# Kernel tuning notes

Hardware: AMD Instinct MI355X
Metric: run time of the kernel (lower is better)

The kernel has to match this reference:

```python
import jax, jax.numpy as jnp
import numpy as np

WINDOW = 11
C1 = 0.01 ** 2
C2 = 0.03 ** 2
PAD = WINDOW // 2


def _box_filter(img, kernel):
    # img: [B,1,H,W], kernel: [1,1,w,w]; SAME padding (odd window)
    return jax.lax.conv_general_dilated(
        img, kernel,
        window_strides=(1, 1),
        padding=[(PAD, PAD), (PAD, PAD)],
        dimension_numbers=('NCHW', 'OIHW', 'NCHW'))


def setup_inputs() -> dict:
    key = jax.random.key(0)
    kx, ky = jax.random.split(key)
    B, C, H, W = 64, 1, 512, 512
    x = jax.random.uniform(kx, (B, C, H, W), dtype=jnp.float32)
    y = jax.random.uniform(ky, (B, C, H, W), dtype=jnp.float32)
    kernel = jnp.ones((1, 1, WINDOW, WINDOW), dtype=jnp.float32) / (WINDOW ** 2)
    return {"x": x, "y": y, "kernel": kernel}


def reference(x, y, kernel):
    mu_x = _box_filter(x, kernel)
    mu_y = _box_filter(y, kernel)
    mu_x2 = mu_x * mu_x
    mu_y2 = mu_y * mu_y
    mu_xy = mu_x * mu_y
    sigma_x2 = _box_filter(x * x, kernel) - mu_x2
    sigma_y2 = _box_filter(y * y, kernel) - mu_y2
    sigma_xy = _box_filter(x * y, kernel) - mu_xy
    ssim_map = ((2.0 * mu_xy + C1) * (2.0 * sigma_xy + C2)) / (
        (mu_x2 + mu_y2 + C1) * (sigma_x2 + sigma_y2 + C2))
    return 1.0 - jnp.mean(ssim_map)
```

## Files before the change

kernel.cpp:

```cpp
#include <hip/hip_runtime.h>
#include <stdint.h>


#define IMG_H 512
#define IMG_W 512
#define N_IMG 64
#define BAND  64
#define NBANDG 8
#define NBLOCKS (N_IMG * NBANDG)
#define NSLOT 19

#define SLOT_BYTES 4128
#define X1_OFF 1040
#define Y0_OFF 2064
#define Y1_OFF 3104

#define C1S2 1.4641f
#define C2S2 13.1769f

typedef __attribute__((address_space(3))) uint32_t lds_u32_t;
typedef const __attribute__((address_space(1))) uint32_t glb_u32_t;

__device__ __forceinline__ void dma16(void* lds, const void* g) {
    __builtin_amdgcn_global_load_lds((glb_u32_t*)g, (lds_u32_t*)lds, 16, 0, 0);
}

__device__ __forceinline__ float dpp_shr1(float v) {
    return __int_as_float(__builtin_amdgcn_update_dpp(
        0, __float_as_int(v), 0x138, 0xF, 0xF, true));
}
__device__ __forceinline__ float dpp_shl1(float v) {
    return __int_as_float(__builtin_amdgcn_update_dpp(
        0, __float_as_int(v), 0x130, 0xF, 0xF, true));
}

__device__ __forceinline__ int wrapS(int s) { return s >= NSLOT ? s - NSLOT : s; }

__global__ __launch_bounds__(128) void ssim_fused(const float* __restrict__ x,
                                                  const float* __restrict__ y,
                                                  float* __restrict__ part)
{
    __shared__ __align__(16) char ring[NSLOT][SLOT_BYTES];

    const int tx = threadIdx.x & 63;
    const int wv = threadIdx.x >> 6;
    const int lo = tx * 32 + ((tx & 32) >> 1);

    const int wid = (blockIdx.x & 7) * (NBLOCKS / 8) + (blockIdx.x >> 3);
    const int img = wid >> 3;
    const int bg  = wid & (NBANDG - 1);
    const int r0  = bg * BAND;

    const float* __restrict__ xi = x + (size_t)img * (IMG_H * IMG_W);
    const float* __restrict__ yi = y + (size_t)img * (IMG_H * IMG_W);

    auto dma_row = [&](int slot, int ri) {
        int rc = ri < 0 ? 0 : (ri > IMG_H - 1 ? IMG_H - 1 : ri);
        char* s = &ring[slot][0];
        const char* xg = (const char*)(xi + (size_t)rc * IMG_W) + tx * 16;
        const char* yg = (const char*)(yi + (size_t)rc * IMG_W) + tx * 16;
        dma16(s,          xg);
        dma16(s + X1_OFF, xg + 1024);
        dma16(s + Y0_OFF, yg);
        dma16(s + Y1_OFF, yg + 1024);
    };

    float Vx[8], Vy[8], Vss[8], Vxy[8];
#pragma unroll
    for (int j = 0; j < 8; ++j) { Vx[j] = 0.f; Vy[j] = 0.f; Vss[j] = 0.f; Vxy[j] = 0.f; }

    auto accum_add = [&](const char* s) {
        const float4* xr = (const float4*)(s + lo);
        const float4* yr = (const float4*)(s + Y0_OFF + lo);
        float4 x0 = xr[0], x1 = xr[1];
        float4 y0 = yr[0], y1 = yr[1];
        float xs[8] = {x0.x, x0.y, x0.z, x0.w, x1.x, x1.y, x1.z, x1.w};
        float ys[8] = {y0.x, y0.y, y0.z, y0.w, y1.x, y1.y, y1.z, y1.w};
#pragma unroll
        for (int j = 0; j < 8; ++j) {
            Vx[j] += xs[j];
            Vy[j] += ys[j];
            Vss[j] = fmaf(xs[j], xs[j], Vss[j]);
            Vss[j] = fmaf(ys[j], ys[j], Vss[j]);
            Vxy[j] = fmaf(xs[j], ys[j], Vxy[j]);
        }
    };

    auto accum_sub = [&](const char* s) {
        const float4* xr = (const float4*)(s + lo);
        const float4* yr = (const float4*)(s + Y0_OFF + lo);
        float4 x0 = xr[0], x1 = xr[1];
        float4 y0 = yr[0], y1 = yr[1];
        float xs[8] = {x0.x, x0.y, x0.z, x0.w, x1.x, x1.y, x1.z, x1.w};
        float ys[8] = {y0.x, y0.y, y0.z, y0.w, y1.x, y1.y, y1.z, y1.w};
#pragma unroll
        for (int j = 0; j < 8; ++j) {
            Vx[j]  -= xs[j];
            Vy[j]  -= ys[j];
            Vss[j] = fmaf(-xs[j], xs[j], Vss[j]);
            Vss[j] = fmaf(-ys[j], ys[j], Vss[j]);
            Vxy[j] = fmaf(-xs[j], ys[j], Vxy[j]);
        }
    };

    auto hsum = [&](const float (&V)[8], float (&S)[8]) {
        float w[18];
#pragma unroll
        for (int k = 0; k < 5; ++k) w[k] = dpp_shr1(V[3 + k]);
#pragma unroll
        for (int j = 0; j < 8; ++j) w[5 + j] = V[j];
#pragma unroll
        for (int k = 0; k < 5; ++k) w[13 + k] = dpp_shl1(V[k]);
        float s0 = (w[0] + w[1]) + (w[2] + w[3]);
        float s1 = (w[4] + w[5]) + (w[6] + w[7]);
        float s2 = (w[8] + w[9]) + w[10];
        float s  = (s0 + s1) + s2;
        S[0] = s;
#pragma unroll
        for (int j = 1; j < 8; ++j) { s += w[j + 10] - w[j - 1]; S[j] = s; }
    };

    auto ssim8 = [&](const float (&Sx)[8], const float (&Sy)[8],
                     const float (&Sss)[8], const float (&Sxy)[8],
                     float& loss) {
#pragma unroll
        for (int j = 0; j < 8; ++j) {
            float A  = Sx[j] * Sy[j];
            float B  = fmaf(Sx[j], Sx[j], Sy[j] * Sy[j]);
            float n1 = fmaf(A, 2.0f, C1S2);
            float n2 = fmaf(Sxy[j], 242.0f, fmaf(A, -2.0f, C2S2));
            float d1 = B + C1S2;
            float d2 = fmaf(Sss[j], 121.0f, C2S2 - B);
            loss += __fdividef(n1 * n2, d1 * d2);
        }
    };

#pragma unroll 1
    for (int k = wv; k < 16; k += 2) dma_row(k, r0 - 7 + k);
    __syncthreads();
#pragma unroll 1
    for (int t = 0; t < 11; ++t) {
        int row = r0 + wv - 7 + t;
        if (row >= 0) accum_add(&ring[wv + t][0]);
    }

    float loss = 0.0f;
    int cA = 11 + wv;
    int cS = wv;
    int cP = 16;
    const int po0 = 1 - wv;
    const int po1 = 3 - wv;

#pragma unroll 1
    for (int i = 0; i < BAND / 4; ++i) {
        const int base = r0 + 4 * i;
        const int a = base + wv;

        if (a + 4 < IMG_H) accum_add(&ring[cA][0]);
        if (a + 5 < IMG_H) accum_add(&ring[wrapS(cA + 1)][0]);
        if (a - 7 >= 0)    accum_sub(&ring[cS][0]);
        if (a - 6 >= 0)    accum_sub(&ring[wrapS(cS + 1)][0]);

        float Sx[8], Sy[8], Sss[8], Sxy[8];
        hsum(Vx, Sx); hsum(Vy, Sy); hsum(Vss, Sss); hsum(Vxy, Sxy);

        if (a + 6 < IMG_H) accum_add(&ring[wrapS(cA + 2)][0]);
        if (a + 7 < IMG_H) accum_add(&ring[wrapS(cA + 3)][0]);
        if (a - 5 >= 0)    accum_sub(&ring[wrapS(cS + 2)][0]);
        if (a - 4 >= 0)    accum_sub(&ring[wrapS(cS + 3)][0]);

        if (i < BAND / 4 - 1) {
            dma_row(wrapS(cP + po0), base + 9 + po0);
            dma_row(wrapS(cP + po1), base + 9 + po1);
        }

        ssim8(Sx, Sy, Sss, Sxy, loss);

        float Tx[8], Ty[8], Tss[8], Txy[8];
        hsum(Vx, Tx); hsum(Vy, Ty); hsum(Vss, Tss); hsum(Vxy, Txy);
        ssim8(Tx, Ty, Tss, Txy, loss);

        cA = wrapS(cA + 4); cS = wrapS(cS + 4); cP = wrapS(cP + 4);
        __syncthreads();
    }

#pragma unroll
    for (int off = 32; off > 0; off >>= 1)
        loss += __shfl_down(loss, off, 64);

    float* pr = reinterpret_cast<float*>(&ring[0][0]);
    if (tx == 0) pr[wv] = loss;
    __syncthreads();
    if (threadIdx.x == 0)
        part[blockIdx.x] = pr[0] + pr[1];
}

__global__ __launch_bounds__(256) void ssim_reduce(const float* __restrict__ part,
                                                   float* __restrict__ out)
{
    const int t  = threadIdx.x;
    const int tx = t & 63;
    float s = part[t] + part[t + 256];
#pragma unroll
    for (int off = 32; off > 0; off >>= 1)
        s += __shfl_down(s, off, 64);
    __shared__ float ws[4];
    if (tx == 0) ws[t >> 6] = s;
    __syncthreads();
    if (t == 0) {
        float total = (ws[0] + ws[1]) + (ws[2] + ws[3]);
        out[0] = 1.0f - total * (1.0f / ((float)N_IMG * IMG_H * IMG_W));
    }
}

extern "C" void kernel_launch(void* const* d_in, const int* in_sizes, int n_in,
                              void* d_out, int out_size, void* d_ws, size_t ws_size,
                              hipStream_t stream) {
    const float* x = (const float*)d_in[0];
    const float* y = (const float*)d_in[1];
    float* part = (float*)d_ws;

    ssim_fused<<<NBLOCKS, 128, 0, stream>>>(x, y, part);
    ssim_reduce<<<1, 256, 0, stream>>>(part, (float*)d_out);
}
```

Measured before the change: 158.2 us.

## Use three wavefronts per block, each advancing one output row per step

The fused SSIM kernel grows from two to three wavefronts per block. Each wave now keeps a separate running column sum for every third row and emits one output row per 3-row step, where before each wave handled two rows per 4-row step. The ring slots lose their padding and the per-lane skew offset, so LDS reads become plain tx*32 strides. The aim is more waves in flight and a simpler schedule; the risks are LDS bank conflicts from the unpadded layout, more redundant add/sub work per output row, and idle waves in the final step.

```diff
diff --git a/kernel.cpp b/kernel.cpp
--- a/kernel.cpp
+++ b/kernel.cpp
@@ -9,11 +9,10 @@
 #define NBANDG 8
 #define NBLOCKS (N_IMG * NBANDG)
 #define NSLOT 19
-
-#define SLOT_BYTES 4128
-#define X1_OFF 1040
-#define Y0_OFF 2064
-#define Y1_OFF 3104
+#define NSTEP 22
+
+#define SLOT_BYTES 4096
+#define Y0_OFF 2048
 
 #define C1S2 1.4641f
 #define C2S2 13.1769f
@@ -36,7 +35,7 @@
 
 __device__ __forceinline__ int wrapS(int s) { return s >= NSLOT ? s - NSLOT : s; }
 
-__global__ __launch_bounds__(128) void ssim_fused(const float* __restrict__ x,
+__global__ __launch_bounds__(192) void ssim_fused(const float* __restrict__ x,
                                                   const float* __restrict__ y,
                                                   float* __restrict__ part)
 {
@@ -44,12 +43,12 @@
 
     const int tx = threadIdx.x & 63;
     const int wv = threadIdx.x >> 6;
-    const int lo = tx * 32 + ((tx & 32) >> 1);
 
     const int wid = (blockIdx.x & 7) * (NBLOCKS / 8) + (blockIdx.x >> 3);
     const int img = wid >> 3;
     const int bg  = wid & (NBANDG - 1);
     const int r0  = bg * BAND;
+    const int q0  = r0 + wv;
 
     const float* __restrict__ xi = x + (size_t)img * (IMG_H * IMG_W);
     const float* __restrict__ yi = y + (size_t)img * (IMG_H * IMG_W);
@@ -60,9 +59,9 @@
         const char* xg = (const char*)(xi + (size_t)rc * IMG_W) + tx * 16;
         const char* yg = (const char*)(yi + (size_t)rc * IMG_W) + tx * 16;
         dma16(s,          xg);
-        dma16(s + X1_OFF, xg + 1024);
+        dma16(s + 1024,   xg + 1024);
         dma16(s + Y0_OFF, yg);
-        dma16(s + Y1_OFF, yg + 1024);
+        dma16(s + Y0_OFF + 1024, yg + 1024);
     };
 
     float Vx[8], Vy[8], Vss[8], Vxy[8];
@@ -70,8 +69,8 @@
     for (int j = 0; j < 8; ++j) { Vx[j] = 0.f; Vy[j] = 0.f; Vss[j] = 0.f; Vxy[j] = 0.f; }
 
     auto accum_add = [&](const char* s) {
-        const float4* xr = (const float4*)(s + lo);
-        const float4* yr = (const float4*)(s + Y0_OFF + lo);
+        const float4* xr = (const float4*)(s + (size_t)tx * 32);
+        const float4* yr = (const float4*)(s + Y0_OFF + (size_t)tx * 32);
         float4 x0 = xr[0], x1 = xr[1];
         float4 y0 = yr[0], y1 = yr[1];
         float xs[8] = {x0.x, x0.y, x0.z, x0.w, x1.x, x1.y, x1.z, x1.w};
@@ -87,8 +86,8 @@
     };
 
     auto accum_sub = [&](const char* s) {
-        const float4* xr = (const float4*)(s + lo);
-        const float4* yr = (const float4*)(s + Y0_OFF + lo);
+        const float4* xr = (const float4*)(s + (size_t)tx * 32);
+        const float4* yr = (const float4*)(s + Y0_OFF + (size_t)tx * 32);
         float4 x0 = xr[0], x1 = xr[1];
         float4 y0 = yr[0], y1 = yr[1];
         float xs[8] = {x0.x, x0.y, x0.z, x0.w, x1.x, x1.y, x1.z, x1.w};
@@ -136,51 +135,41 @@
     };
 
 #pragma unroll 1
-    for (int k = wv; k < 16; k += 2) dma_row(k, r0 - 7 + k);
+    for (int k = wv; k < 16; k += 3) dma_row(k + 1, r0 - 8 + k);
     __syncthreads();
 #pragma unroll 1
     for (int t = 0; t < 11; ++t) {
-        int row = r0 + wv - 7 + t;
-        if (row >= 0) accum_add(&ring[wv + t][0]);
+        int row = q0 - 8 + t;
+        if (row >= 0) accum_add(&ring[wv + 1 + t][0]);
     }
 
     float loss = 0.0f;
-    int cA = 11 + wv;
-    int cS = wv;
-    int cP = 16;
-    const int po0 = 1 - wv;
-    const int po1 = 3 - wv;
+    int c = 0;
 
 #pragma unroll 1
-    for (int i = 0; i < BAND / 4; ++i) {
-        const int base = r0 + 4 * i;
-        const int a = base + wv;
-
-        if (a + 4 < IMG_H) accum_add(&ring[cA][0]);
-        if (a + 5 < IMG_H) accum_add(&ring[wrapS(cA + 1)][0]);
-        if (a - 7 >= 0)    accum_sub(&ring[cS][0]);
-        if (a - 6 >= 0)    accum_sub(&ring[wrapS(cS + 1)][0]);
-
-        float Sx[8], Sy[8], Sss[8], Sxy[8];
-        hsum(Vx, Sx); hsum(Vy, Sy); hsum(Vss, Sss); hsum(Vxy, Sxy);
-
-        if (a + 6 < IMG_H) accum_add(&ring[wrapS(cA + 2)][0]);
-        if (a + 7 < IMG_H) accum_add(&ring[wrapS(cA + 3)][0]);
-        if (a - 5 >= 0)    accum_sub(&ring[wrapS(cS + 2)][0]);
-        if (a - 4 >= 0)    accum_sub(&ring[wrapS(cS + 3)][0]);
-
-        if (i < BAND / 4 - 1) {
-            dma_row(wrapS(cP + po0), base + 9 + po0);
-            dma_row(wrapS(cP + po1), base + 9 + po1);
-        }
-
-        ssim8(Sx, Sy, Sss, Sxy, loss);
-
-        float Tx[8], Ty[8], Tss[8], Txy[8];
-        hsum(Vx, Tx); hsum(Vy, Ty); hsum(Vss, Tss); hsum(Vxy, Txy);
-        ssim8(Tx, Ty, Tss, Txy, loss);
-
-        cA = wrapS(cA + 4); cS = wrapS(cS + 4); cP = wrapS(cP + 4);
+    for (int i = 0; i < NSTEP; ++i) {
+        const int base = r0 + 3 * i;
+        const int q = base + wv;
+        const bool act = (3 * i + wv) < BAND;
+
+        if (act) {
+            if (q - 8 >= 0) accum_sub(&ring[wrapS(c + 1 + wv)][0]);
+            if (q - 7 >= 0) accum_sub(&ring[wrapS(c + 2 + wv)][0]);
+            if (q - 6 >= 0) accum_sub(&ring[wrapS(c + 3 + wv)][0]);
+            if (q + 3 < IMG_H) accum_add(&ring[wrapS(c + 12 + wv)][0]);
+            if (q + 4 < IMG_H) accum_add(&ring[wrapS(c + 13 + wv)][0]);
+            if (q + 5 < IMG_H) accum_add(&ring[wrapS(c + 14 + wv)][0]);
+        }
+
+        if (i < NSTEP - 1) dma_row(wrapS(c + 17 + wv), base + 8 + wv);
+
+        if (act) {
+            float Sx[8], Sy[8], Sss[8], Sxy[8];
+            hsum(Vx, Sx); hsum(Vy, Sy); hsum(Vss, Sss); hsum(Vxy, Sxy);
+            ssim8(Sx, Sy, Sss, Sxy, loss);
+        }
+
+        c = wrapS(c + 3);
         __syncthreads();
     }
 
@@ -192,7 +181,7 @@
     if (tx == 0) pr[wv] = loss;
     __syncthreads();
     if (threadIdx.x == 0)
-        part[blockIdx.x] = pr[0] + pr[1];
+        part[blockIdx.x] = (pr[0] + pr[1]) + pr[2];
 }
 
 __global__ __launch_bounds__(256) void ssim_reduce(const float* __restrict__ part,
@@ -220,6 +209,6 @@
     const float* y = (const float*)d_in[1];
     float* part = (float*)d_ws;
 
-    ssim_fused<<<NBLOCKS, 128, 0, stream>>>(x, y, part);
+    ssim_fused<<<NBLOCKS, 192, 0, stream>>>(x, y, part);
     ssim_reduce<<<1, 256, 0, stream>>>(part, (float*)d_out);
 }
```

New measurement: 166.9 us. +5.5%, slower.
